# Optimization experiments

Measured on AMD Instinct MI355X. Metric: run time of the kernel, lower is better.

## Reference

```python
import jax, jax.numpy as jnp
import numpy as np
import math

IMG_SIZE = 768
NUM_CLASSES = 90
THRESHOLD = 0.05
IOU_THRESHOLD = 0.5
MAX_DETECTIONS = 100
K_CAND = 512  # per-class candidate pool before greedy NMS
RATIOS = [(1.0, 1.0), (1.4, 0.7), (0.7, 1.4)]
SCALES = [2 ** 0, 2 ** (1.0 / 3.0), 2 ** (2.0 / 3.0)]


def _generate_anchors():
    anchor_scale = 4.0
    pyramid_levels = [3, 4, 5, 6, 7]
    all_levels = []
    for lv in pyramid_levels:
        stride = 2 ** lv
        size = anchor_scale * 2 ** lv
        grid = IMG_SIZE // stride
        sx = np.arange(grid) * stride
        sy, sx = np.meshgrid(np.arange(grid) * stride, sx, indexing='ij')
        # torch meshgrid(shift_y, shift_x, indexing='ij') -> rows are y
        yy, xx = np.meshgrid(np.arange(grid) * stride, np.arange(grid) * stride, indexing='ij')
        shifts = np.stack([xx.ravel(), yy.ravel(), xx.ravel(), yy.ravel()], axis=1).astype(np.float32)
        base = []
        for r in RATIOS:
            for s in SCALES:
                w = size * s * math.sqrt(r[0] / r[1])
                h = size * s * math.sqrt(r[1] / r[0])
                base.append([-w / 2, -h / 2, w / 2, h / 2])
        base = np.asarray(base, dtype=np.float32)  # [9,4]
        anc = (base[None, :, :] + shifts[:, None, :]).reshape(-1, 4)
        all_levels.append(anc)
    return np.concatenate(all_levels, axis=0)  # [110484,4]


def setup_inputs() -> dict:
    key = jax.random.key(0)
    k1, k2, k3 = jax.random.split(key, 3)
    A = 110484
    x = jax.random.normal(k1, (1, 3, IMG_SIZE, IMG_SIZE), dtype=jnp.float32)
    regression = jax.random.normal(k2, (1, A, 4), dtype=jnp.float32) * 0.3
    classification = jax.random.normal(k3, (1, A, NUM_CLASSES), dtype=jnp.float32) - 2.0
    anchors = jnp.asarray(_generate_anchors())
    return {"x": x, "regression": regression, "classification": classification, "anchors": anchors}


def _decode_and_clip(anchors, deltas, H, W):
    # BBoxTransform (RetinaNet-style): deltas = (dx, dy, dw, dh)
    wa = anchors[:, 2] - anchors[:, 0]
    ha = anchors[:, 3] - anchors[:, 1]
    cxa = anchors[:, 0] + 0.5 * wa
    cya = anchors[:, 1] + 0.5 * ha
    dx, dy, dw, dh = deltas[:, 0], deltas[:, 1], deltas[:, 2], deltas[:, 3]
    cx = cxa + dx * wa
    cy = cya + dy * ha
    w = jnp.exp(dw) * wa
    h = jnp.exp(dh) * ha
    x1 = jnp.clip(cx - 0.5 * w, 0.0, W)
    y1 = jnp.clip(cy - 0.5 * h, 0.0, H)
    x2 = jnp.clip(cx + 0.5 * w, 0.0, W)
    y2 = jnp.clip(cy + 0.5 * h, 0.0, H)
    return jnp.stack([x1, y1, x2, y2], axis=1)  # [A,4]


def _pairwise_iou(b):  # [K,4] -> [K,K]
    area = (b[:, 2] - b[:, 0]) * (b[:, 3] - b[:, 1])
    xx1 = jnp.maximum(b[:, None, 0], b[None, :, 0])
    yy1 = jnp.maximum(b[:, None, 1], b[None, :, 1])
    xx2 = jnp.minimum(b[:, None, 2], b[None, :, 2])
    yy2 = jnp.minimum(b[:, None, 3], b[None, :, 3])
    inter = jnp.clip(xx2 - xx1, 0.0) * jnp.clip(yy2 - yy1, 0.0)
    return inter / (area[:, None] + area[None, :] - inter + 1e-8)


def _greedy_nms(iou_c, valid_c):
    # boxes are pre-sorted by descending score; fixed-iteration greedy NMS
    def step(suppressed, i):
        keep_i = valid_c[i] & jnp.logical_not(suppressed[i])
        suppressed = jnp.where(keep_i, suppressed | (iou_c[i] > IOU_THRESHOLD), suppressed)
        return suppressed, keep_i
    _, keep = jax.lax.scan(step, jnp.zeros(iou_c.shape[0], dtype=bool), jnp.arange(iou_c.shape[0]))
    return keep  # [K]


def _postprocess(x, regression, classification, anchors):
    H, W = x.shape[2], x.shape[3]
    boxes = _decode_and_clip(anchors, regression[0], float(H), float(W))  # [A,4]
    scores = jax.nn.sigmoid(classification[0])                            # [A,C]
    # per-class top-K candidate pool (sorted desc), fixed-shape NMS
    vals, idx = jax.lax.top_k(scores.T, K_CAND)        # [C,K]
    cand = boxes[idx]                                   # [C,K,4]
    valid = vals > THRESHOLD                            # [C,K]
    iou = jax.vmap(_pairwise_iou)(cand)                 # [C,K,K]
    keep = jax.vmap(_greedy_nms)(iou, valid)            # [C,K]
    kept_scores = jnp.where(keep, vals, -1.0).reshape(-1)  # [C*K]
    top_vals, flat_idx = jax.lax.top_k(kept_scores, MAX_DETECTIONS)
    labels = (flat_idx // K_CAND).astype(jnp.float32)
    det_boxes = cand.reshape(-1, 4)[flat_idx]
    ok = top_vals > 0.0
    det = jnp.concatenate([
        jnp.zeros((MAX_DETECTIONS, 1), dtype=jnp.float32),  # batch ids (batch=1 -> 0)
        det_boxes,
        top_vals[:, None],
        labels[:, None],
    ], axis=1)  # [100,7]
    return jnp.where(ok[:, None], det, 0.0)


def reference(x, regression, classification, anchors):
    return _postprocess(x, regression, classification, anchors)
```

## Files before the change

kernel.cpp:

```cpp
#include <hip/hip_runtime.h>
#include <math.h>


#define A_N   110484
#define C_N   90
#define KCAND 512
#define NBINS 8192
#define KSH   19
#define MAXDET 100
#define IMG_F 768.0f
#define THRESH 0.05f
#define NS    4
#define VTOT  (A_N / 4)
#define VS4   ((VTOT + NS - 1) / NS)
#define SL_CAP 1024
#define CAND_N (NS * KCAND)
#define KEEP_CAP 100
#define T_BLKS ((A_N + 63) / 64)
#define S_BLKS (C_N * NS)
#define SEL_T 512
#define D_BLKS ((A_N + SEL_T - 1) / SEL_T)
#define FCAP  512

typedef unsigned int u32;
typedef unsigned long long u64;

__device__ __forceinline__ u32 fkey(float f) {
    u32 u = __float_as_uint(f);
    return (u & 0x80000000u) ? ~u : (u | 0x80000000u);
}
__device__ __forceinline__ float unfkey(u32 k) {
    u32 u = (k & 0x80000000u) ? (k ^ 0x80000000u) : ~k;
    return __uint_as_float(u);
}
__device__ __forceinline__ u64 shflx64(u64 v, int m) {
    u32 lo = (u32)__shfl_xor((int)(u32)v, m, 64);
    u32 hi = (u32)__shfl_xor((int)(v >> 32), m, 64);
    return ((u64)hi << 32) | lo;
}

__global__ __launch_bounds__(256)
void prep_kernel(const float* __restrict__ cls,
                 u32* __restrict__ keysT) {
    __shared__ u32 tile[64 * 91];
    const int a0 = blockIdx.x * 64;
    const int lim = min(64, A_N - a0);
    const int n4 = (lim * C_N) >> 2;
    const float4* src4 = (const float4*)(cls + (size_t)a0 * C_N);
    for (int i4 = threadIdx.x; i4 < n4; i4 += 256) {
        float4 x4 = src4[i4];
        const u32 base = (u32)(4 * i4);
        float xs[4] = { x4.x, x4.y, x4.z, x4.w };
        #pragma unroll
        for (int k = 0; k < 4; ++k) {
            u32 i = base + k;
            u32 aa = i / C_N, c = i % C_N;
            float s = 1.0f / (1.0f + expf(-xs[k]));
            tile[aa * 91 + c] = fkey(s);
        }
    }
    __syncthreads();
    for (int j = threadIdx.x; j < C_N * 64; j += 256) {
        int c = j >> 6, aa = j & 63;
        if (aa < lim)
            keysT[(size_t)c * A_N + a0 + aa] = tile[aa * 91 + c];
    }
}

__global__ __launch_bounds__(SEL_T)
void select_kernel(const u32* __restrict__ keysT,
                   const float* __restrict__ anchors,
                   const float* __restrict__ reg,
                   float4* __restrict__ boxes,
                   u64* __restrict__ candbuf) {
    __shared__ u32 hist[NBINS / 2];
    __shared__ u32 csum[SEL_T];
    __shared__ u64 lbuf[SL_CAP];
    __shared__ u32 sPv;
    __shared__ int lcnt;
    const int tid = threadIdx.x;

    if (blockIdx.x >= S_BLKS) {
        int a = (blockIdx.x - S_BLKS) * SEL_T + tid;
        if (a < A_N) {
            float4 an = ((const float4*)anchors)[a];
            float4 dl = ((const float4*)reg)[a];
            float wa = an.z - an.x, ha = an.w - an.y;
            float cx = an.x + 0.5f * wa + dl.x * wa;
            float cy = an.y + 0.5f * ha + dl.y * ha;
            float w = expf(dl.z) * wa;
            float h = expf(dl.w) * ha;
            float4 o;
            o.x = fminf(fmaxf(cx - 0.5f * w, 0.0f), IMG_F);
            o.y = fminf(fmaxf(cy - 0.5f * h, 0.0f), IMG_F);
            o.z = fminf(fmaxf(cx + 0.5f * w, 0.0f), IMG_F);
            o.w = fminf(fmaxf(cy + 0.5f * h, 0.0f), IMG_F);
            boxes[a] = o;
        }
        return;
    }
    const int c = blockIdx.x >> 2, s = blockIdx.x & 3;
    const int lo = s * VS4, hiEnd = min(VTOT, lo + VS4);
    const uint4* kv = (const uint4*)(keysT + (size_t)c * A_N);

    for (int i = tid; i < NBINS / 2; i += SEL_T) hist[i] = 0;
    if (tid == 0) { sPv = 0; lcnt = 0; }
    __syncthreads();

    #define HACC(K) do { \
        u32 b0 = (K).x >> KSH, b1 = (K).y >> KSH, b2 = (K).z >> KSH, b3 = (K).w >> KSH; \
        atomicAdd(&hist[b0 >> 1], 1u << ((b0 & 1) << 4)); \
        atomicAdd(&hist[b1 >> 1], 1u << ((b1 & 1) << 4)); \
        atomicAdd(&hist[b2 >> 1], 1u << ((b2 & 1) << 4)); \
        atomicAdd(&hist[b3 >> 1], 1u << ((b3 & 1) << 4)); } while (0)
    {
        int i = lo + tid;
        for (; i + 3 * SEL_T < hiEnd; i += 4 * SEL_T) {
            uint4 ka = kv[i], kb = kv[i + SEL_T], kc = kv[i + 2 * SEL_T], kd = kv[i + 3 * SEL_T];
            HACC(ka); HACC(kb); HACC(kc); HACC(kd);
        }
        for (; i < hiEnd; i += SEL_T) { uint4 ka = kv[i]; HACC(ka); }
    }
    __syncthreads();

    u32 own = 0;
    {
        const int wb = (NBINS / 2) - 8 - 8 * tid;
        const int g = (tid >> 2) & 7;
        #pragma unroll
        for (int jj = 0; jj < 8; ++jj) {
            u32 v = hist[wb + ((g + jj) & 7)];
            own += (v & 0xffffu) + (v >> 16);
        }
    }
    csum[tid] = own;
    __syncthreads();
    for (int off = 1; off < SEL_T; off <<= 1) {
        u32 v = csum[tid];
        u32 a = (tid >= off) ? csum[tid - off] : 0u;
        __syncthreads();
        csum[tid] = v + a;
        __syncthreads();
    }
    const u32 incl = csum[tid], excl = incl - own;
    if (excl < (u32)KCAND && incl >= (u32)KCAND) {
        u32 cum = excl;
        const int hb = NBINS - 1 - 16 * tid;
        for (int j = 0; j < 16; ++j) {
            int b = hb - j;
            u32 v = hist[b >> 1];
            u32 cnt = (b & 1) ? (v >> 16) : (v & 0xffffu);
            if (cum + cnt >= (u32)KCAND) { sPv = (u32)b; break; }
            cum += cnt;
        }
    }
    __syncthreads();
    const u32 P = sPv;

    #define CACC(K, BASE) do { \
        if (((K).x >> KSH) >= P) { int p = atomicAdd(&lcnt, 1); if (p < SL_CAP) lbuf[p] = (((u64)(~(K).x)) << 32) | (u32)(BASE); } \
        if (((K).y >> KSH) >= P) { int p = atomicAdd(&lcnt, 1); if (p < SL_CAP) lbuf[p] = (((u64)(~(K).y)) << 32) | (u32)((BASE) + 1); } \
        if (((K).z >> KSH) >= P) { int p = atomicAdd(&lcnt, 1); if (p < SL_CAP) lbuf[p] = (((u64)(~(K).z)) << 32) | (u32)((BASE) + 2); } \
        if (((K).w >> KSH) >= P) { int p = atomicAdd(&lcnt, 1); if (p < SL_CAP) lbuf[p] = (((u64)(~(K).w)) << 32) | (u32)((BASE) + 3); } } while (0)
    {
        int i = lo + tid;
        for (; i + 3 * SEL_T < hiEnd; i += 4 * SEL_T) {
            uint4 ka = kv[i], kb = kv[i + SEL_T], kc = kv[i + 2 * SEL_T], kd = kv[i + 3 * SEL_T];
            CACC(ka, 4 * i); CACC(kb, 4 * (i + SEL_T)); CACC(kc, 4 * (i + 2 * SEL_T)); CACC(kd, 4 * (i + 3 * SEL_T));
        }
        for (; i < hiEnd; i += SEL_T) { uint4 ka = kv[i]; CACC(ka, 4 * i); }
    }
    __syncthreads();
    const int n = min(lcnt, SL_CAP);
    for (int q = tid; q < SL_CAP; q += SEL_T) if (q >= n) lbuf[q] = ~0ULL;
    __syncthreads();

    {
        const int l = tid & 63, w = tid >> 6;
        const int i0 = 128 * w + l, i1 = i0 + 64;
        u64 v0 = lbuf[i0], v1 = lbuf[i1];
        __syncthreads();
        #pragma unroll
        for (u32 kk = 2; kk <= 1024; kk <<= 1) {
            #pragma unroll
            for (u32 j = kk >> 1; j > 0; j >>= 1) {
                if (j >= 128) {
                    lbuf[i0] = v0; lbuf[i1] = v1;
                    __syncthreads();
                    u64 w0 = lbuf[i0 ^ j], w1 = lbuf[i1 ^ j];
                    bool m0 = (((i0 & j) == 0) == ((i0 & kk) == 0));
                    bool m1 = (((i1 & j) == 0) == ((i1 & kk) == 0));
                    v0 = m0 ? (v0 < w0 ? v0 : w0) : (v0 > w0 ? v0 : w0);
                    v1 = m1 ? (v1 < w1 ? v1 : w1) : (v1 > w1 ? v1 : w1);
                    __syncthreads();
                } else if (j == 64) {
                    bool up = ((i0 & kk) == 0);
                    u64 mn = v0 < v1 ? v0 : v1, mx = v0 < v1 ? v1 : v0;
                    v0 = up ? mn : mx; v1 = up ? mx : mn;
                } else {
                    u64 w0 = shflx64(v0, (int)j), w1 = shflx64(v1, (int)j);
                    bool m0 = (((i0 & j) == 0) == ((i0 & kk) == 0));
                    bool m1 = (((i1 & j) == 0) == ((i1 & kk) == 0));
                    v0 = m0 ? (v0 < w0 ? v0 : w0) : (v0 > w0 ? v0 : w0);
                    v1 = m1 ? (v1 < w1 ? v1 : w1) : (v1 > w1 ? v1 : w1);
                }
            }
        }
        if (w < 4) {
            u64* cb = candbuf + (size_t)c * CAND_N + (size_t)s * KCAND;
            const bool rev = (s & 1);
            int d0 = rev ? (KCAND - 1 - i0) : i0;
            int d1 = rev ? (KCAND - 1 - i1) : i1;
            cb[d0] = v0; cb[d1] = v1;
        }
    }
}

__global__ __launch_bounds__(1024)
void nms_kernel(const u64* __restrict__ candbuf,
                const float4* __restrict__ boxes,
                u32* __restrict__ keptbuf, u32* __restrict__ cnt2) {
    __shared__ u64 sortbuf[2][CAND_N];
    __shared__ float bxx[KCAND], byy[KCAND], bzz[KCAND], bww[KCAND];
    __shared__ float ar[KCAND], sc[KCAND];
    __shared__ u32 keepf[16], wbase[17];
    u32* bmask = (u32*)&sortbuf[0][0];
    const int c = blockIdx.x, tid = threadIdx.x;
    const int l = tid & 63, w = tid >> 6;
    const int i0 = 128 * w + l, i1 = i0 + 64;

    const u64* cb = candbuf + (size_t)c * CAND_N;
    u64 v0 = cb[i0], v1 = cb[i1];
    int p = 0;
    #pragma unroll
    for (u32 kk = 1024; kk <= (u32)CAND_N; kk <<= 1) {
        #pragma unroll
        for (u32 j = kk >> 1; j > 0; j >>= 1) {
            if (j >= 128) {
                sortbuf[p][i0] = v0; sortbuf[p][i1] = v1;
                __syncthreads();
                u64 w0 = sortbuf[p][i0 ^ j], w1 = sortbuf[p][i1 ^ j];
                bool m0 = (((i0 & j) == 0) == ((i0 & kk) == 0));
                bool m1 = (((i1 & j) == 0) == ((i1 & kk) == 0));
                v0 = m0 ? (v0 < w0 ? v0 : w0) : (v0 > w0 ? v0 : w0);
                v1 = m1 ? (v1 < w1 ? v1 : w1) : (v1 > w1 ? v1 : w1);
                p ^= 1;
            } else if (j == 64) {
                bool up = ((i0 & kk) == 0);
                u64 mn = v0 < v1 ? v0 : v1, mx = v0 < v1 ? v1 : v0;
                v0 = up ? mn : mx; v1 = up ? mx : mn;
            } else {
                u64 w0 = shflx64(v0, (int)j), w1 = shflx64(v1, (int)j);
                bool m0 = (((i0 & j) == 0) == ((i0 & kk) == 0));
                bool m1 = (((i1 & j) == 0) == ((i1 & kk) == 0));
                v0 = m0 ? (v0 < w0 ? v0 : w0) : (v0 > w0 ? v0 : w0);
                v1 = m1 ? (v1 < w1 ? v1 : w1) : (v1 > w1 ? v1 : w1);
            }
        }
    }
    __syncthreads();

    if (w < 4) {
        u32 idx0 = (u32)v0, key0 = ~((u32)(v0 >> 32));
        u32 idx1 = (u32)v1, key1 = ~((u32)(v1 >> 32));
        sc[i0] = unfkey(key0); sc[i1] = unfkey(key1);
        float4 b0 = boxes[idx0], b1 = boxes[idx1];
        bxx[i0] = b0.x; byy[i0] = b0.y; bzz[i0] = b0.z; bww[i0] = b0.w;
        bxx[i1] = b1.x; byy[i1] = b1.y; bzz[i1] = b1.z; bww[i1] = b1.w;
        ar[i0] = (b0.z - b0.x) * (b0.w - b0.y);
        ar[i1] = (b1.z - b1.x) * (b1.w - b1.y);
    }
    if (tid < 16) keepf[tid] = 0;
    __syncthreads();

    for (int r = w; r < KCAND; r += 16) {
        const float bix = bxx[r], biy = byy[r], biz = bzz[r], biw = bww[r];
        const float ai = ar[r];
        const int q0 = (r + 1) >> 6;
        u32* row = bmask + r * 16;
        if (l < 2 * q0) row[l] = 0;
        for (int q = q0; q < 8; ++q) {
            const int j = q * 64 + l;
            float xx1 = fmaxf(bix, bxx[j]), yy1 = fmaxf(biy, byy[j]);
            float xx2 = fminf(biz, bzz[j]), yy2 = fminf(biw, bww[j]);
            float inter = fmaxf(xx2 - xx1, 0.0f) * fmaxf(yy2 - yy1, 0.0f);
            float uni = ai + ar[j] - inter + 1e-8f;
            bool sup = (j > r) && (inter > 0.5f * uni);
            u64 bal = __ballot(sup);
            if (l == 0)      row[2 * q]     = (u32)bal;
            else if (l == 1) row[2 * q + 1] = (u32)(bal >> 32);
        }
    }
    __syncthreads();

    if (tid < 64) {
        const int lw = tid & 15;
        u32 removed = 0, keepw = 0;
        u32 rA[8], rB[8]; float sA[8], sB[8];
        #pragma unroll
        for (int k = 0; k < 8; ++k) { rA[k] = bmask[k * 16 + lw]; sA[k] = sc[k]; }
        #pragma unroll 1
        for (int ch = 0; ch < 64; ch += 2) {
            const int tb1 = (ch + 1) * 8;
            #pragma unroll
            for (int k = 0; k < 8; ++k) { rB[k] = bmask[(tb1 + k) * 16 + lw]; sB[k] = sc[tb1 + k]; }
            {
                const int tb = ch * 8;
                #pragma unroll
                for (int k = 0; k < 8; ++k) {
                    const int t = tb + k;
                    u32 rw = (u32)__builtin_amdgcn_readlane((int)removed, t >> 5);
                    bool d = (sA[k] > THRESH) && (((rw >> (t & 31)) & 1u) == 0u);
                    removed |= d ? rA[k] : 0u;
                    keepw |= (d && (tid == (t >> 5))) ? (1u << (t & 31)) : 0u;
                }
            }
            const int tb2 = (ch + 2 < 64) ? (ch + 2) * 8 : 0;
            #pragma unroll
            for (int k = 0; k < 8; ++k) { rA[k] = bmask[(tb2 + k) * 16 + lw]; sA[k] = sc[tb2 + k]; }
            {
                #pragma unroll
                for (int k = 0; k < 8; ++k) {
                    const int t = tb1 + k;
                    u32 rw = (u32)__builtin_amdgcn_readlane((int)removed, t >> 5);
                    bool d = (sB[k] > THRESH) && (((rw >> (t & 31)) & 1u) == 0u);
                    removed |= d ? rB[k] : 0u;
                    keepw |= (d && (tid == (t >> 5))) ? (1u << (t & 31)) : 0u;
                }
            }
        }
        if (tid < 16) keepf[tid] = keepw;
    }
    __syncthreads();

    if (tid == 0) {
        u32 t = 0;
        for (int q = 0; q < 16; ++q) { wbase[q] = t; t += __popc(keepf[q]); }
        wbase[16] = t;
        cnt2[c] = (t < (u32)KEEP_CAP) ? t : (u32)KEEP_CAP;
    }
    __syncthreads();
    if (tid < KCAND) {
        u32 word = keepf[tid >> 5];
        u32 bit = (u32)tid & 31u;
        if ((word >> bit) & 1u) {
            u32 rank = wbase[tid >> 5] + __popc(word & ((1u << bit) - 1u));
            if (rank < (u32)KEEP_CAP) {
                float s = sc[tid];
                uint4 a, b;
                a.x = ~fkey(s);
                a.y = (u32)(c * KCAND + tid);
                a.z = __float_as_uint(bxx[tid]);
                a.w = __float_as_uint(byy[tid]);
                b.x = __float_as_uint(bzz[tid]);
                b.y = __float_as_uint(bww[tid]);
                b.z = __float_as_uint(s);
                b.w = 0u;
                uint4* e = (uint4*)(keptbuf + ((size_t)c * KEEP_CAP + rank) * 8);
                e[0] = a; e[1] = b;
            }
        }
    }
}

__global__ __launch_bounds__(1024)
void final_kernel(const u32* __restrict__ keptbuf, const u32* __restrict__ cnt2,
                  float* __restrict__ out) {
    __shared__ u32 hist[NBINS];
    __shared__ u32 csum[1024];
    __shared__ u64 ebuf[FCAP];
    __shared__ u32 eidx[FCAP];
    __shared__ u32 scnt[C_N];
    __shared__ u32 sP;
    __shared__ int sN;
    const int tid = threadIdx.x;
    const int TOT = C_N * KEEP_CAP;

    for (int i = tid; i < MAXDET * 7; i += 1024) out[i] = 0.0f;
    for (int i = tid; i < NBINS; i += 1024) hist[i] = 0;
    if (tid < C_N) scnt[tid] = cnt2[tid];
    if (tid == 0) { sN = 0; sP = NBINS - 1; }
    __syncthreads();

    for (int i = tid; i < TOT; i += 1024) {
        u32 c = (u32)i / KEEP_CAP, pp = (u32)i % KEEP_CAP;
        if (pp < scnt[c]) {
            u32 khi = keptbuf[(size_t)i * 8];
            atomicAdd(&hist[khi >> KSH], 1u);
        }
    }
    __syncthreads();
    u32 own = 0; const int lo = 8 * tid;
    #pragma unroll
    for (int j = 0; j < 8; ++j) own += hist[lo + j];
    csum[tid] = own;
    __syncthreads();
    for (int off = 1; off < 1024; off <<= 1) {
        u32 v = csum[tid];
        u32 a = (tid >= off) ? csum[tid - off] : 0u;
        __syncthreads();
        csum[tid] = v + a;
        __syncthreads();
    }
    const u32 incl = csum[tid], excl = incl - own;
    if (excl < (u32)MAXDET && incl >= (u32)MAXDET) {
        u32 cum = excl;
        for (int j = 0; j < 8; ++j) {
            u32 h = hist[lo + j];
            if (cum + h >= (u32)MAXDET) { sP = (u32)(lo + j); break; }
            cum += h;
        }
    }
    __syncthreads();
    const u32 P = sP;
    for (int i = tid; i < TOT; i += 1024) {
        u32 c = (u32)i / KEEP_CAP, pp = (u32)i % KEEP_CAP;
        if (pp < scnt[c]) {
            const uint2 v2 = *((const uint2*)(keptbuf + (size_t)i * 8));
            if ((v2.x >> KSH) <= P) {
                int p = atomicAdd(&sN, 1);
                if (p < FCAP) {
                    ebuf[p] = ((u64)v2.x << 32) | v2.y;
                    eidx[p] = (u32)i;
                }
            }
        }
    }
    __syncthreads();
    const int n = min(sN, FCAP);
    u32 m = 128; while ((int)m < n) m <<= 1;
    for (int i = tid; i < (int)m; i += 1024) if (i >= n) ebuf[i] = ~0ULL;
    __syncthreads();
    for (u32 kk = 2; kk <= m; kk <<= 1) {
        for (u32 j = kk >> 1; j > 0; j >>= 1) {
            u32 i = (u32)tid;
            if (i < m) {
                u32 ixj = i ^ j;
                if (ixj > i) {
                    u64 x = ebuf[i], y = ebuf[ixj];
                    bool up = ((i & kk) == 0);
                    if (up ? (x > y) : (x < y)) {
                        ebuf[i] = y; ebuf[ixj] = x;
                        u32 t = eidx[i]; eidx[i] = eidx[ixj]; eidx[ixj] = t;
                    }
                }
            }
            __syncthreads();
        }
    }
    if (tid < MAXDET && tid < n) {
        u64 comp = ebuf[tid];
        if (comp != ~0ULL) {
            const uint4* e = (const uint4*)(keptbuf + (size_t)eidx[tid] * 8);
            uint4 a = e[0], b = e[1];
            float* o = out + tid * 7;
            o[0] = 0.0f;
            o[1] = __uint_as_float(a.z); o[2] = __uint_as_float(a.w);
            o[3] = __uint_as_float(b.x); o[4] = __uint_as_float(b.y);
            o[5] = __uint_as_float(b.z);
            o[6] = (float)(((u32)comp) >> 9);
        }
    }
}

extern "C" void kernel_launch(void* const* d_in, const int* in_sizes, int n_in,
                              void* d_out, int out_size, void* d_ws, size_t ws_size,
                              hipStream_t stream) {
    const float* reg     = (const float*)d_in[1];
    const float* cls     = (const float*)d_in[2];
    const float* anchors = (const float*)d_in[3];
    float* out = (float*)d_out;

    char* ws = (char*)d_ws;
    size_t off = 0;
    auto alloc = [&](size_t bytes) -> void* {
        void* p = ws + off;
        off = (off + bytes + 255) & ~(size_t)255;
        return p;
    };
    u32*    keysT   = (u32*)   alloc((size_t)C_N * A_N * sizeof(u32));
    float4* boxes   = (float4*)alloc((size_t)A_N * sizeof(float4));
    u64*    candbuf = (u64*)   alloc((size_t)C_N * CAND_N * sizeof(u64));
    u32*    keptbuf = (u32*)   alloc((size_t)C_N * KEEP_CAP * 8 * sizeof(u32));
    u32*    cnt2    = (u32*)   alloc((size_t)C_N * sizeof(u32));
    (void)ws_size;

    prep_kernel<<<T_BLKS, 256, 0, stream>>>(cls, keysT);
    select_kernel<<<S_BLKS + D_BLKS, SEL_T, 0, stream>>>(keysT, anchors, reg, boxes, candbuf);
    nms_kernel<<<C_N, 1024, 0, stream>>>(candbuf, boxes, keptbuf, cnt2);
    final_kernel<<<1, 1024, 0, stream>>>(keptbuf, cnt2, out);
}
```

Baseline: 210.0 us.

## Pack boxes as float4, cache column boxes in registers, early-exit greedy NMS

The NMS kernel now stores candidate boxes as packed float4 in shared memory. Each lane keeps its eight column boxes and their areas in registers across all rows, so the IoU bitmask pass no longer reloads them from LDS, and each 64-bit ballot is written with one store. The greedy scan gains a wave-wide popcount check that stops once KEEP_CAP boxes are kept. It also sets launch_bounds min-blocks to 4, which may force register limits or spills.

```diff
diff --git a/kernel.cpp b/kernel.cpp
--- a/kernel.cpp
+++ b/kernel.cpp
@@ -216,13 +216,13 @@
     }
 }
 
-__global__ __launch_bounds__(1024)
+__global__ __launch_bounds__(1024, 4)
 void nms_kernel(const u64* __restrict__ candbuf,
                 const float4* __restrict__ boxes,
                 u32* __restrict__ keptbuf, u32* __restrict__ cnt2) {
     __shared__ u64 sortbuf[2][CAND_N];
-    __shared__ float bxx[KCAND], byy[KCAND], bzz[KCAND], bww[KCAND];
-    __shared__ float ar[KCAND], sc[KCAND];
+    __shared__ float4 bb4[KCAND];
+    __shared__ float sc[KCAND];
     __shared__ u32 keepf[16], wbase[17];
     u32* bmask = (u32*)&sortbuf[0][0];
     const int c = blockIdx.x, tid = threadIdx.x;
@@ -264,32 +264,48 @@
         u32 idx0 = (u32)v0, key0 = ~((u32)(v0 >> 32));
         u32 idx1 = (u32)v1, key1 = ~((u32)(v1 >> 32));
         sc[i0] = unfkey(key0); sc[i1] = unfkey(key1);
-        float4 b0 = boxes[idx0], b1 = boxes[idx1];
-        bxx[i0] = b0.x; byy[i0] = b0.y; bzz[i0] = b0.z; bww[i0] = b0.w;
-        bxx[i1] = b1.x; byy[i1] = b1.y; bzz[i1] = b1.z; bww[i1] = b1.w;
-        ar[i0] = (b0.z - b0.x) * (b0.w - b0.y);
-        ar[i1] = (b1.z - b1.x) * (b1.w - b1.y);
+        bb4[i0] = boxes[idx0]; bb4[i1] = boxes[idx1];
     }
     if (tid < 16) keepf[tid] = 0;
     __syncthreads();
 
-    for (int r = w; r < KCAND; r += 16) {
-        const float bix = bxx[r], biy = byy[r], biz = bzz[r], biw = bww[r];
-        const float ai = ar[r];
-        const int q0 = (r + 1) >> 6;
-        u32* row = bmask + r * 16;
-        if (l < 2 * q0) row[l] = 0;
-        for (int q = q0; q < 8; ++q) {
-            const int j = q * 64 + l;
-            float xx1 = fmaxf(bix, bxx[j]), yy1 = fmaxf(biy, byy[j]);
-            float xx2 = fminf(biz, bzz[j]), yy2 = fminf(biw, bww[j]);
-            float inter = fmaxf(xx2 - xx1, 0.0f) * fmaxf(yy2 - yy1, 0.0f);
-            float uni = ai + ar[j] - inter + 1e-8f;
-            bool sup = (j > r) && (inter > 0.5f * uni);
-            u64 bal = __ballot(sup);
-            if (l == 0)      row[2 * q]     = (u32)bal;
-            else if (l == 1) row[2 * q + 1] = (u32)(bal >> 32);
-        }
+    {
+        const float4 cj0 = bb4[0 * 64 + l], cj1 = bb4[1 * 64 + l];
+        const float4 cj2 = bb4[2 * 64 + l], cj3 = bb4[3 * 64 + l];
+        const float4 cj4 = bb4[4 * 64 + l], cj5 = bb4[5 * 64 + l];
+        const float4 cj6 = bb4[6 * 64 + l], cj7 = bb4[7 * 64 + l];
+        const float aj0 = (cj0.z - cj0.x) * (cj0.w - cj0.y);
+        const float aj1 = (cj1.z - cj1.x) * (cj1.w - cj1.y);
+        const float aj2 = (cj2.z - cj2.x) * (cj2.w - cj2.y);
+        const float aj3 = (cj3.z - cj3.x) * (cj3.w - cj3.y);
+        const float aj4 = (cj4.z - cj4.x) * (cj4.w - cj4.y);
+        const float aj5 = (cj5.z - cj5.x) * (cj5.w - cj5.y);
+        const float aj6 = (cj6.z - cj6.x) * (cj6.w - cj6.y);
+        const float aj7 = (cj7.z - cj7.x) * (cj7.w - cj7.y);
+
+        #define QSTEP(QQ, CJ, AJ) do { \
+            if (QQ >= q0) { \
+                float xx1 = fmaxf(bi.x, (CJ).x), yy1 = fmaxf(bi.y, (CJ).y); \
+                float xx2 = fminf(bi.z, (CJ).z), yy2 = fminf(bi.w, (CJ).w); \
+                float inter = fmaxf(xx2 - xx1, 0.0f) * fmaxf(yy2 - yy1, 0.0f); \
+                float uni = ai + (AJ) - inter + 1e-8f; \
+                bool sup = ((QQ * 64 + l) > r) && (inter > 0.5f * uni); \
+                u64 bal = __ballot(sup); \
+                if (l == 0) *(u64*)(row + 2 * QQ) = bal; \
+            } } while (0)
+
+        for (int r = w; r < KCAND; r += 16) {
+            const float4 bi = bb4[r];
+            const float ai = (bi.z - bi.x) * (bi.w - bi.y);
+            const int q0 = (r + 1) >> 6;
+            u32* row = bmask + r * 16;
+            if (l < 2 * q0) row[l] = 0;
+            QSTEP(0, cj0, aj0); QSTEP(1, cj1, aj1);
+            QSTEP(2, cj2, aj2); QSTEP(3, cj3, aj3);
+            QSTEP(4, cj4, aj4); QSTEP(5, cj5, aj5);
+            QSTEP(6, cj6, aj6); QSTEP(7, cj7, aj7);
+        }
+        #undef QSTEP
     }
     __syncthreads();
 
@@ -328,6 +344,10 @@
                     keepw |= (d && (tid == (t >> 5))) ? (1u << (t & 31)) : 0u;
                 }
             }
+            u32 cnt = (u32)__popc(keepw);
+            #pragma unroll
+            for (int m = 32; m; m >>= 1) cnt += (u32)__shfl_xor((int)cnt, m, 64);
+            if (cnt >= (u32)KEEP_CAP) break;
         }
         if (tid < 16) keepf[tid] = keepw;
     }
@@ -347,17 +367,18 @@
             u32 rank = wbase[tid >> 5] + __popc(word & ((1u << bit) - 1u));
             if (rank < (u32)KEEP_CAP) {
                 float s = sc[tid];
-                uint4 a, b;
-                a.x = ~fkey(s);
-                a.y = (u32)(c * KCAND + tid);
-                a.z = __float_as_uint(bxx[tid]);
-                a.w = __float_as_uint(byy[tid]);
-                b.x = __float_as_uint(bzz[tid]);
-                b.y = __float_as_uint(bww[tid]);
-                b.z = __float_as_uint(s);
-                b.w = 0u;
+                float4 b = bb4[tid];
+                uint4 a2, b2;
+                a2.x = ~fkey(s);
+                a2.y = (u32)(c * KCAND + tid);
+                a2.z = __float_as_uint(b.x);
+                a2.w = __float_as_uint(b.y);
+                b2.x = __float_as_uint(b.z);
+                b2.y = __float_as_uint(b.w);
+                b2.z = __float_as_uint(s);
+                b2.w = 0u;
                 uint4* e = (uint4*)(keptbuf + ((size_t)c * KEEP_CAP + rank) * 8);
-                e[0] = a; e[1] = b;
+                e[0] = a2; e[1] = b2;
             }
         }
     }
```

Result: faster. 184.2 us (-12.3%).
